# Kernel optimization log

Hardware: AMD Instinct MI355X
Metric: run time of the kernel (lower is better)

The kernel has to match this reference:

```python
import jax, jax.numpy as jnp
import numpy as np

NUM_SPARSE = 26
VOCAB = 100000
EMB = 64
B = 2048
DENSE = 13
NUM_FEA = NUM_SPARSE + 1  # 26 embeddings + bottom-MLP output


def _xavier(key, shape):
    fan_in, fan_out = shape[0], shape[1]
    lim = jnp.sqrt(6.0 / (fan_in + fan_out))
    return jax.random.uniform(key, shape, jnp.float32, -lim, lim)


def setup_inputs() -> dict:
    key = jax.random.key(0)
    ks = jax.random.split(key, 20)
    inp = {
        "dense": jax.random.normal(ks[0], (B, DENSE), jnp.float32),
        "cat_idx": jax.random.randint(ks[1], (B, NUM_SPARSE), 0, VOCAB, jnp.int32),
        # stacked EmbeddingBag tables (all same vocab -> one [26, V, 64] tensor)
        "tables": _xavier(ks[2], (VOCAB, EMB))[None] * jnp.ones((NUM_SPARSE, 1, 1), jnp.float32) * 0
                  + jax.random.normal(ks[3], (NUM_SPARSE, VOCAB, EMB), jnp.float32) * 0.01,
        # bottom MLP: 13 -> 512 -> 256 -> 64
        "bw0": _xavier(ks[4], (DENSE, 512)), "bb0": jnp.zeros((512,), jnp.float32),
        "bw1": _xavier(ks[5], (512, 256)),   "bb1": jnp.zeros((256,), jnp.float32),
        "bw2": _xavier(ks[6], (256, EMB)),   "bb2": jnp.zeros((EMB,), jnp.float32),
        # top MLP: 415 -> 1024 -> 512 -> 256 -> 1
        "tw0": _xavier(ks[7], (EMB + NUM_FEA * (NUM_FEA - 1) // 2, 1024)), "tb0": jnp.zeros((1024,), jnp.float32),
        "tw1": _xavier(ks[8], (1024, 512)),  "tb1": jnp.zeros((512,), jnp.float32),
        "tw2": _xavier(ks[9], (512, 256)),   "tb2": jnp.zeros((256,), jnp.float32),
        "tw3": _xavier(ks[10], (256, 1)),    "tb3": jnp.zeros((1,), jnp.float32),
    }
    return inp


def reference(dense, cat_idx, tables, bw0, bb0, bw1, bb1, bw2, bb2,
              tw0, tb0, tw1, tb1, tw2, tb2, tw3, tb3):
    # bottom MLP on dense features -> [B, EMB]
    h = jax.nn.relu(dense @ bw0 + bb0)
    h = jax.nn.relu(h @ bw1 + bb1)
    bot = jax.nn.relu(h @ bw2 + bb2)

    # EmbeddingBag (single index per bag, sum mode == plain gather): [B, 26, EMB]
    feat_ids = jnp.arange(NUM_SPARSE)[None, :]  # [1, 26]
    emb = tables[feat_ids, cat_idx]             # [B, 26, EMB]

    # dot interaction: batched Gram matrix then lower-triangular gather
    T = jnp.concatenate([bot[:, None, :], emb], axis=1)  # [B, 27, EMB]
    Z = jnp.einsum("bif,bjf->bij", T, T)                  # [B, 27, 27]
    li, lj = np.tril_indices(NUM_FEA, k=-1)               # 351 pairs
    Zflat = Z[:, li, lj]                                  # [B, 351]

    R = jnp.concatenate([bot, Zflat], axis=1)             # [B, 415]

    # top MLP
    r = jax.nn.relu(R @ tw0 + tb0)
    r = jax.nn.relu(r @ tw1 + tb1)
    r = jax.nn.relu(r @ tw2 + tb2)
    out = jax.nn.sigmoid(r @ tw3 + tb3)                   # [B, 1]
    return out
```

## Files before the change

kernel.cpp:

```cpp
#include <hip/hip_runtime.h>
#include <hip/hip_bf16.h>


#define BATCH 2048
#define VOCAB 100000
#define NSPARSE 26
#define NFEA 27
#define NPAIR 351
#define RLD 512

typedef __attribute__((ext_vector_type(8))) __bf16 bf16x8;
typedef __attribute__((ext_vector_type(4))) float f32x4;
typedef __hip_bfloat16 bf16;

#define GLOAD16(g, l)                                                          \
    __builtin_amdgcn_global_load_lds(                                          \
        (const __attribute__((address_space(1))) unsigned int*)(g),            \
        (__attribute__((address_space(3))) unsigned int*)(l), 16, 0, 0)

template<int BK>
__device__ __forceinline__ int swz(int row, int s) {
    return (BK == 128) ? (s ^ (row & 15))
         : (BK == 64)  ? (s ^ (row & 7))
                       : (s ^ ((row >> 1) & 3));
}

template<int BK, int WR, int WC, int MREP, int NREP, bool DENSEPAD>
__global__ __launch_bounds__(256) void gemm_bf16(
    const void* __restrict__ Araw,
    const bf16* __restrict__ Wt,
    const float* __restrict__ bias,
    bf16* __restrict__ C,
    int M, int N, int K, int ldC)
{
    constexpr int BM    = WR * MREP * 16;
    constexpr int BN    = WC * NREP * 16;
    constexpr int ROWB  = BK * 2;
    constexpr int SLOTS = BK / 8;
    constexpr int KKS   = BK / 32;
    constexpr int PA    = BM * SLOTS / 256;
    constexpr int PB    = BN * SLOTS / 256;

    __shared__ __align__(16) bf16 As[BM * BK];
    __shared__ __align__(16) bf16 Bs[BN * BK];

    const int t   = threadIdx.x;
    const int nbn = N / BN;
    const int bm  = blockIdx.x / nbn;
    const int bn  = blockIdx.x % nbn;
    const int row0 = bm * BM, n0 = bn * BN;

    const int wid  = t >> 6, lane = t & 63;
    const int wr   = wid / WC, wc = wid % WC;
    const int lr   = lane & 15;
    const int q    = lane >> 4;
    const int sslot = t % SLOTS;

    const bf16* Ab[PA];
    const bf16* Bb[PB];
#pragma unroll
    for (int p = 0; p < PA; ++p) {
        const int r = (p * 256 + t) / SLOTS;
        if (!DENSEPAD)
            Ab[p] = (const bf16*)Araw + (size_t)(row0 + r) * K +
                    swz<BK>(r, sslot) * 8;
    }
#pragma unroll
    for (int p = 0; p < PB; ++p) {
        const int r = (p * 256 + t) / SLOTS;
        Bb[p] = Wt + (size_t)(n0 + r) * K + swz<BK>(r, sslot) * 8;
    }

    f32x4 acc[MREP][NREP] = {};

    for (int k0 = 0; k0 < K; k0 += BK) {
        if constexpr (DENSEPAD) {
            const float* Df = (const float*)Araw;
#pragma unroll
            for (int idx = t; idx < BM * 32; idx += 256) {
                const int r = idx >> 5, c = idx & 31;
                const float v = (c < 13) ? Df[(size_t)(row0 + r) * 13 + c] : 0.f;
                As[r * 32 + swz<32>(r, c >> 3) * 8 + (c & 7)] =
                    __float2bfloat16(v);
            }
        } else {
#pragma unroll
            for (int p = 0; p < PA; ++p)
                GLOAD16(Ab[p] + k0, (char*)As + (p * 256 + t) * 16);
        }
#pragma unroll
        for (int p = 0; p < PB; ++p)
            GLOAD16(Bb[p] + k0, (char*)Bs + (p * 256 + t) * 16);
        __syncthreads();

        bf16x8 af[KKS][MREP], bfr[KKS][NREP];
#pragma unroll
        for (int kk = 0; kk < KKS; ++kk) {
#pragma unroll
            for (int m = 0; m < MREP; ++m) {
                const int r = wr * MREP * 16 + 16 * m + lr;
                af[kk][m] = *(const bf16x8*)((const char*)As + r * ROWB +
                                             swz<BK>(r, kk * 4 + q) * 16);
            }
#pragma unroll
            for (int n = 0; n < NREP; ++n) {
                const int r = wc * NREP * 16 + 16 * n + lr;
                bfr[kk][n] = *(const bf16x8*)((const char*)Bs + r * ROWB +
                                              swz<BK>(r, kk * 4 + q) * 16);
            }
        }
#pragma unroll
        for (int kk = 0; kk < KKS; ++kk)
#pragma unroll
            for (int m = 0; m < MREP; ++m)
#pragma unroll
                for (int n = 0; n < NREP; ++n)
                    acc[m][n] = __builtin_amdgcn_mfma_f32_16x16x32_bf16(
                        af[kk][m], bfr[kk][n], acc[m][n], 0, 0, 0);
        __syncthreads();
    }

#pragma unroll
    for (int n = 0; n < NREP; ++n) {
        const int col = n0 + wc * NREP * 16 + 16 * n + lr;
        const float bv = bias[col];
#pragma unroll
        for (int m = 0; m < MREP; ++m) {
#pragma unroll
            for (int i = 0; i < 4; ++i) {
                const int row = row0 + wr * MREP * 16 + 16 * m + q * 4 + i;
                float v = fmaxf(acc[m][n][i] + bv, 0.f);
                C[(size_t)row * ldC + col] = __float2bfloat16(v);
            }
        }
    }
}

__global__ __launch_bounds__(256) void top2_kernel(
    const bf16* __restrict__ A,
    const bf16* __restrict__ Wt,
    const float* __restrict__ bias,
    const float* __restrict__ w3,
    const float* __restrict__ b3,
    float* __restrict__ out)
{
    constexpr int BK = 64, BM = 32, K = 512;
    constexpr int SLOTS = 8, KKS = 2, PA = 1, PB = 8;

    __shared__ __align__(16) bf16 As[BM * BK];
    __shared__ __align__(16) bf16 Bs[256 * BK];
    __shared__ float rsum[BM];

    const int t = threadIdx.x;
    const int row0 = blockIdx.x * BM;
    const int wc = t >> 6, lane = t & 63;
    const int lr = lane & 15, q = lane >> 4;
    const int sslot = t % SLOTS;

    const bf16* Ab[PA];
    const bf16* Bb[PB];
#pragma unroll
    for (int p = 0; p < PA; ++p) {
        const int r = (p * 256 + t) / SLOTS;
        Ab[p] = A + (size_t)(row0 + r) * K + swz<BK>(r, sslot) * 8;
    }
#pragma unroll
    for (int p = 0; p < PB; ++p) {
        const int r = (p * 256 + t) / SLOTS;
        Bb[p] = Wt + (size_t)r * K + swz<BK>(r, sslot) * 8;
    }

    f32x4 acc[2][4] = {};

    for (int k0 = 0; k0 < K; k0 += BK) {
#pragma unroll
        for (int p = 0; p < PA; ++p)
            GLOAD16(Ab[p] + k0, (char*)As + (p * 256 + t) * 16);
#pragma unroll
        for (int p = 0; p < PB; ++p)
            GLOAD16(Bb[p] + k0, (char*)Bs + (p * 256 + t) * 16);
        __syncthreads();

        bf16x8 af[KKS][2], bfr[KKS][4];
#pragma unroll
        for (int kk = 0; kk < KKS; ++kk) {
#pragma unroll
            for (int m = 0; m < 2; ++m) {
                const int r = 16 * m + lr;
                af[kk][m] = *(const bf16x8*)((const char*)As + r * 128 +
                                             swz<BK>(r, kk * 4 + q) * 16);
            }
#pragma unroll
            for (int n = 0; n < 4; ++n) {
                const int r = wc * 64 + 16 * n + lr;
                bfr[kk][n] = *(const bf16x8*)((const char*)Bs + r * 128 +
                                              swz<BK>(r, kk * 4 + q) * 16);
            }
        }
#pragma unroll
        for (int kk = 0; kk < KKS; ++kk)
#pragma unroll
            for (int m = 0; m < 2; ++m)
#pragma unroll
                for (int n = 0; n < 4; ++n)
                    acc[m][n] = __builtin_amdgcn_mfma_f32_16x16x32_bf16(
                        af[kk][m], bfr[kk][n], acc[m][n], 0, 0, 0);
        __syncthreads();
    }

    if (t < BM) rsum[t] = 0.f;
    __syncthreads();

#pragma unroll
    for (int m = 0; m < 2; ++m) {
#pragma unroll
        for (int i = 0; i < 4; ++i) {
            float val = 0.f;
#pragma unroll
            for (int n = 0; n < 4; ++n) {
                const int col = wc * 64 + 16 * n + lr;
                val += fmaxf(acc[m][n][i] + bias[col], 0.f) * w3[col];
            }
            val += __shfl_xor(val, 1);
            val += __shfl_xor(val, 2);
            val += __shfl_xor(val, 4);
            val += __shfl_xor(val, 8);
            if (lr == 0) atomicAdd(&rsum[16 * m + q * 4 + i], val);
        }
    }
    __syncthreads();
    if (t < BM)
        out[row0 + t] = 1.f / (1.f + expf(-(rsum[t] + b3[0])));
}

struct WConvArgs {
    const float* src[6];
    bf16*        dst[6];
    int K[6], N[6], Kp[6], t0[7];
};

__global__ __launch_bounds__(256) void wconv_kernel(WConvArgs a)
{
    __shared__ float Ts[32][33];
    int w = 0;
    while (w < 5 && (int)blockIdx.x >= a.t0[w + 1]) ++w;
    const int rel = blockIdx.x - a.t0[w];
    const int K = a.K[w], N = a.N[w], Kp = a.Kp[w];
    const int nbn = N >> 5;
    const int tk = rel / nbn, tn = rel % nbn;
    const int tx = threadIdx.x & 31, ty = threadIdx.x >> 5;

    const float* src = a.src[w];
    bf16* dst = a.dst[w];

#pragma unroll
    for (int rr = 0; rr < 4; ++rr) {
        const int k = tk * 32 + ty + rr * 8;
        const int n = tn * 32 + tx;
        Ts[ty + rr * 8][tx] = (k < K) ? src[(size_t)k * N + n] : 0.f;
    }
    __syncthreads();
#pragma unroll
    for (int rr = 0; rr < 4; ++rr) {
        const int n = tn * 32 + ty + rr * 8;
        const int kp = tk * 32 + tx;
        dst[(size_t)n * Kp + kp] = __float2bfloat16(Ts[tx][ty + rr * 8]);
    }
}

__global__ __launch_bounds__(256) void interact_kernel(
    const int* __restrict__ cat_idx, const float* __restrict__ tables,
    bf16* __restrict__ R)
{
    __shared__ float T[NFEA][64 + 1];

    const int b    = blockIdx.x;
    const int t    = threadIdx.x;
    const int g    = t >> 6;
    const int lane = t & 63;
    bf16* Rrow = R + (size_t)b * RLD;

    for (int f = g; f < NFEA; f += 4) {
        if (f == 0) {
            T[0][lane] = __bfloat162float(Rrow[lane]);
        } else {
            const int j   = f - 1;
            const int idx = cat_idx[b * NSPARSE + j];
            T[f][lane] = tables[((size_t)j * VOCAB + idx) * 64 + lane];
        }
    }
    __syncthreads();

    if (t < RLD - 415) Rrow[415 + t] = __float2bfloat16(0.f);

    for (int p = t; p < NPAIR; p += 256) {
        int i = (int)((1.0f + sqrtf(1.0f + 8.0f * (float)p)) * 0.5f);
        while (i * (i - 1) / 2 > p) --i;
        while ((i + 1) * i / 2 <= p) ++i;
        const int j = p - i * (i - 1) / 2;
        float s = 0.f;
#pragma unroll 16
        for (int k = 0; k < 64; ++k) s += T[i][k] * T[j][k];
        Rrow[64 + p] = __float2bfloat16(s);
    }
}

extern "C" void kernel_launch(void* const* d_in, const int* in_sizes, int n_in,
                              void* d_out, int out_size, void* d_ws, size_t ws_size,
                              hipStream_t stream)
{
    const float* dense   = (const float*)d_in[0];
    const int*   cat_idx = (const int*)  d_in[1];
    const float* tables  = (const float*)d_in[2];
    const float* bw0 = (const float*)d_in[3];
    const float* bb0 = (const float*)d_in[4];
    const float* bw1 = (const float*)d_in[5];
    const float* bb1 = (const float*)d_in[6];
    const float* bw2 = (const float*)d_in[7];
    const float* bb2 = (const float*)d_in[8];
    const float* tw0 = (const float*)d_in[9];
    const float* tb0 = (const float*)d_in[10];
    const float* tw1 = (const float*)d_in[11];
    const float* tb1 = (const float*)d_in[12];
    const float* tw2 = (const float*)d_in[13];
    const float* tb2 = (const float*)d_in[14];
    const float* tw3 = (const float*)d_in[15];
    const float* tb3 = (const float*)d_in[16];

    bf16* p = (bf16*)d_ws;
    bf16* h0   = p; p += (size_t)BATCH * 512;
    bf16* h1   = p; p += (size_t)BATCH * 256;
    bf16* R    = p; p += (size_t)BATCH * RLD;
    bf16* r0   = p; p += (size_t)BATCH * 1024;
    bf16* r1   = p; p += (size_t)BATCH * 512;
    bf16* bw0t = p; p += 512 * 32;
    bf16* bw1t = p; p += 256 * 512;
    bf16* bw2t = p; p += 64 * 256;
    bf16* tw0t = p; p += 1024 * RLD;
    bf16* tw1t = p; p += 512 * 1024;
    bf16* tw2t = p; p += 256 * 512;
    float* out = (float*)d_out;

    WConvArgs wa;
    wa.src[0] = bw0;  wa.dst[0] = bw0t; wa.K[0] = 13;   wa.N[0] = 512;  wa.Kp[0] = 32;
    wa.src[1] = bw1;  wa.dst[1] = bw1t; wa.K[1] = 512;  wa.N[1] = 256;  wa.Kp[1] = 512;
    wa.src[2] = bw2;  wa.dst[2] = bw2t; wa.K[2] = 256;  wa.N[2] = 64;   wa.Kp[2] = 256;
    wa.src[3] = tw0;  wa.dst[3] = tw0t; wa.K[3] = 415;  wa.N[3] = 1024; wa.Kp[3] = RLD;
    wa.src[4] = tw1;  wa.dst[4] = tw1t; wa.K[4] = 1024; wa.N[4] = 512;  wa.Kp[4] = 1024;
    wa.src[5] = tw2;  wa.dst[5] = tw2t; wa.K[5] = 512;  wa.N[5] = 256;  wa.Kp[5] = 512;
    int tiles = 0;
    for (int w = 0; w < 6; ++w) {
        wa.t0[w] = tiles;
        tiles += (wa.Kp[w] >> 5) * (wa.N[w] >> 5);
    }
    wa.t0[6] = tiles;

    wconv_kernel<<<tiles, 256, 0, stream>>>(wa);

    gemm_bf16<32, 2, 2, 2, 2, true ><<<(BATCH / 64) * (512 / 64), 256, 0, stream>>>(
        dense, bw0t, bb0, h0, BATCH, 512, 32, 512);
    gemm_bf16<128, 2, 2, 1, 2, false><<<(BATCH / 32) * (256 / 64), 256, 0, stream>>>(
        h0, bw1t, bb1, h1, BATCH, 256, 512, 256);
    gemm_bf16<128, 2, 2, 1, 2, false><<<(BATCH / 32) * (64 / 64), 256, 0, stream>>>(
        h1, bw2t, bb2, R, BATCH, 64, 256, RLD);

    interact_kernel<<<BATCH, 256, 0, stream>>>(cat_idx, tables, R);

    gemm_bf16<128, 2, 2, 2, 2, false><<<(BATCH / 64) * (1024 / 64), 256, 0, stream>>>(
        R, tw0t, tb0, r0, BATCH, 1024, RLD, 1024);
    gemm_bf16<128, 2, 2, 1, 2, false><<<(BATCH / 32) * (512 / 64), 256, 0, stream>>>(
        r0, tw1t, tb1, r1, BATCH, 512, 1024, 512);
    top2_kernel<<<BATCH / 32, 256, 0, stream>>>(r1, tw2t, tb2, tw3, tb3, out);
}
```

Before: 59.70 us.

## Fuse three bottom-MLP GEMMs into one kernel keeping activations in LDS

Replaces the three separate bottom-MLP GEMM launches with a single kernel. Each block handles 8 batch rows, padded to 16 for MFMA, and keeps the intermediate activations h0 and h1 in swizzled shared memory, so they are never written to or read from global memory. This removes two kernel launches and the global round-trips of the intermediates. In exchange, half of each MFMA row tile is wasted on padding, and weights are read straight from global memory in every one of 256 blocks instead of being staged through LDS tiles.

```diff
diff --git a/kernel.cpp b/kernel.cpp
--- a/kernel.cpp
+++ b/kernel.cpp
@@ -13,6 +13,8 @@
 typedef __attribute__((ext_vector_type(4))) float f32x4;
 typedef __hip_bfloat16 bf16;
 
+#define MFMA16 __builtin_amdgcn_mfma_f32_16x16x32_bf16
+
 #define GLOAD16(g, l)                                                          \
     __builtin_amdgcn_global_load_lds(                                          \
         (const __attribute__((address_space(1))) unsigned int*)(g),            \
@@ -25,12 +27,115 @@
                        : (s ^ ((row >> 1) & 3));
 }
 
-template<int BK, int WR, int WC, int MREP, int NREP, bool DENSEPAD>
+__global__ __launch_bounds__(256) void bottom_kernel(
+    const float* __restrict__ dense,
+    const bf16* __restrict__ bw0t, const float* __restrict__ bb0,
+    const bf16* __restrict__ bw1t, const float* __restrict__ bb1,
+    const bf16* __restrict__ bw2t, const float* __restrict__ bb2,
+    bf16* __restrict__ R)
+{
+    __shared__ __align__(16) bf16 ds[16 * 32];
+    __shared__ __align__(16) bf16 h0s[16 * 512];
+    __shared__ __align__(16) bf16 h1s[16 * 256];
+
+    const int t   = threadIdx.x;
+    const int b0  = blockIdx.x * 8;
+    const int wid = t >> 6, lane = t & 63;
+    const int lr  = lane & 15, q = lane >> 4;
+
+    for (int idx = t; idx < 16 * 32; idx += 256) {
+        const int r = idx >> 5, c = idx & 31;
+        const float v = (r < 8 && c < 13) ? dense[(size_t)(b0 + r) * 13 + c] : 0.f;
+        ds[r * 32 + swz<32>(r, c >> 3) * 8 + (c & 7)] = __float2bfloat16(v);
+    }
+    __syncthreads();
+
+    {
+        const bf16x8 af = *(const bf16x8*)&ds[lr * 32 + swz<32>(lr, q) * 8];
+        const int n0 = wid * 128;
+        f32x4 acc[8] = {};
+#pragma unroll
+        for (int n = 0; n < 8; ++n) {
+            const bf16x8 bv =
+                *(const bf16x8*)(bw0t + (size_t)(n0 + n * 16 + lr) * 32 + q * 8);
+            acc[n] = MFMA16(af, bv, acc[n], 0, 0, 0);
+        }
+#pragma unroll
+        for (int n = 0; n < 8; ++n) {
+            const int col = n0 + n * 16 + lr;
+            const float bv = bb0[col];
+#pragma unroll
+            for (int i = 0; i < 4; ++i) {
+                const int row = q * 4 + i;
+                const float v = fmaxf(acc[n][i] + bv, 0.f);
+                h0s[row * 512 + (((col >> 3) ^ (row & 15)) << 3) + (col & 7)] =
+                    __float2bfloat16(v);
+            }
+        }
+    }
+    __syncthreads();
+
+    {
+        const int n0 = wid * 64;
+        const bf16* wp[4];
+#pragma unroll
+        for (int n = 0; n < 4; ++n)
+            wp[n] = bw1t + (size_t)(n0 + n * 16 + lr) * 512 + q * 8;
+
+        f32x4 acc[4] = {};
+#pragma unroll 4
+        for (int kk = 0; kk < 16; ++kk) {
+            const bf16x8 af = *(const bf16x8*)
+                &h0s[lr * 512 + (((kk * 4 + q) ^ (lr & 15)) << 3)];
+#pragma unroll
+            for (int n = 0; n < 4; ++n) {
+                const bf16x8 bv = *(const bf16x8*)(wp[n] + kk * 32);
+                acc[n] = MFMA16(af, bv, acc[n], 0, 0, 0);
+            }
+        }
+#pragma unroll
+        for (int n = 0; n < 4; ++n) {
+            const int col = n0 + n * 16 + lr;
+            const float bv = bb1[col];
+#pragma unroll
+            for (int i = 0; i < 4; ++i) {
+                const int row = q * 4 + i;
+                const float v = fmaxf(acc[n][i] + bv, 0.f);
+                h1s[row * 256 + (((col >> 3) ^ (row & 15)) << 3) + (col & 7)] =
+                    __float2bfloat16(v);
+            }
+        }
+    }
+    __syncthreads();
+
+    {
+        const int n0 = wid * 16;
+        const bf16* wp = bw2t + (size_t)(n0 + lr) * 256 + q * 8;
+        f32x4 acc = {};
+#pragma unroll
+        for (int kk = 0; kk < 8; ++kk) {
+            const bf16x8 af = *(const bf16x8*)
+                &h1s[lr * 256 + (((kk * 4 + q) ^ (lr & 15)) << 3)];
+            const bf16x8 bv = *(const bf16x8*)(wp + kk * 32);
+            acc = MFMA16(af, bv, acc, 0, 0, 0);
+        }
+        const int col = n0 + lr;
+        const float bv = bb2[col];
+#pragma unroll
+        for (int i = 0; i < 4; ++i) {
+            const int row = q * 4 + i;
+            if (row < 8) {
+                const float v = fmaxf(acc[i] + bv, 0.f);
+                R[(size_t)(b0 + row) * RLD + col] = __float2bfloat16(v);
+            }
+        }
+    }
+}
+
+template<int BK, int WR, int WC, int MREP, int NREP>
 __global__ __launch_bounds__(256) void gemm_bf16(
-    const void* __restrict__ Araw,
-    const bf16* __restrict__ Wt,
-    const float* __restrict__ bias,
-    bf16* __restrict__ C,
+    const bf16* __restrict__ A, const bf16* __restrict__ Wt,
+    const float* __restrict__ bias, bf16* __restrict__ C,
     int M, int N, int K, int ldC)
 {
     constexpr int BM    = WR * MREP * 16;
@@ -61,9 +166,7 @@
 #pragma unroll
     for (int p = 0; p < PA; ++p) {
         const int r = (p * 256 + t) / SLOTS;
-        if (!DENSEPAD)
-            Ab[p] = (const bf16*)Araw + (size_t)(row0 + r) * K +
-                    swz<BK>(r, sslot) * 8;
+        Ab[p] = A + (size_t)(row0 + r) * K + swz<BK>(r, sslot) * 8;
     }
 #pragma unroll
     for (int p = 0; p < PB; ++p) {
@@ -74,20 +177,9 @@
     f32x4 acc[MREP][NREP] = {};
 
     for (int k0 = 0; k0 < K; k0 += BK) {
-        if constexpr (DENSEPAD) {
-            const float* Df = (const float*)Araw;
-#pragma unroll
-            for (int idx = t; idx < BM * 32; idx += 256) {
-                const int r = idx >> 5, c = idx & 31;
-                const float v = (c < 13) ? Df[(size_t)(row0 + r) * 13 + c] : 0.f;
-                As[r * 32 + swz<32>(r, c >> 3) * 8 + (c & 7)] =
-                    __float2bfloat16(v);
-            }
-        } else {
-#pragma unroll
-            for (int p = 0; p < PA; ++p)
-                GLOAD16(Ab[p] + k0, (char*)As + (p * 256 + t) * 16);
-        }
+#pragma unroll
+        for (int p = 0; p < PA; ++p)
+            GLOAD16(Ab[p] + k0, (char*)As + (p * 256 + t) * 16);
 #pragma unroll
         for (int p = 0; p < PB; ++p)
             GLOAD16(Bb[p] + k0, (char*)Bs + (p * 256 + t) * 16);
@@ -115,8 +207,7 @@
             for (int m = 0; m < MREP; ++m)
 #pragma unroll
                 for (int n = 0; n < NREP; ++n)
-                    acc[m][n] = __builtin_amdgcn_mfma_f32_16x16x32_bf16(
-                        af[kk][m], bfr[kk][n], acc[m][n], 0, 0, 0);
+                    acc[m][n] = MFMA16(af[kk][m], bfr[kk][n], acc[m][n], 0, 0, 0);
         __syncthreads();
     }
 
@@ -137,12 +228,9 @@
 }
 
 __global__ __launch_bounds__(256) void top2_kernel(
-    const bf16* __restrict__ A,
-    const bf16* __restrict__ Wt,
-    const float* __restrict__ bias,
-    const float* __restrict__ w3,
-    const float* __restrict__ b3,
-    float* __restrict__ out)
+    const bf16* __restrict__ A, const bf16* __restrict__ Wt,
+    const float* __restrict__ bias, const float* __restrict__ w3,
+    const float* __restrict__ b3, float* __restrict__ out)
 {
     constexpr int BK = 64, BM = 32, K = 512;
     constexpr int SLOTS = 8, KKS = 2, PA = 1, PB = 8;
@@ -203,8 +291,7 @@
             for (int m = 0; m < 2; ++m)
 #pragma unroll
                 for (int n = 0; n < 4; ++n)
-                    acc[m][n] = __builtin_amdgcn_mfma_f32_16x16x32_bf16(
-                        af[kk][m], bfr[kk][n], acc[m][n], 0, 0, 0);
+                    acc[m][n] = MFMA16(af[kk][m], bfr[kk][n], acc[m][n], 0, 0, 0);
         __syncthreads();
     }
 
@@ -328,8 +415,6 @@
     const float* tb3 = (const float*)d_in[16];
 
     bf16* p = (bf16*)d_ws;
-    bf16* h0   = p; p += (size_t)BATCH * 512;
-    bf16* h1   = p; p += (size_t)BATCH * 256;
     bf16* R    = p; p += (size_t)BATCH * RLD;
     bf16* r0   = p; p += (size_t)BATCH * 1024;
     bf16* r1   = p; p += (size_t)BATCH * 512;
@@ -357,18 +442,14 @@
 
     wconv_kernel<<<tiles, 256, 0, stream>>>(wa);
 
-    gemm_bf16<32, 2, 2, 2, 2, true ><<<(BATCH / 64) * (512 / 64), 256, 0, stream>>>(
-        dense, bw0t, bb0, h0, BATCH, 512, 32, 512);
-    gemm_bf16<128, 2, 2, 1, 2, false><<<(BATCH / 32) * (256 / 64), 256, 0, stream>>>(
-        h0, bw1t, bb1, h1, BATCH, 256, 512, 256);
-    gemm_bf16<128, 2, 2, 1, 2, false><<<(BATCH / 32) * (64 / 64), 256, 0, stream>>>(
-        h1, bw2t, bb2, R, BATCH, 64, 256, RLD);
+    bottom_kernel<<<BATCH / 8, 256, 0, stream>>>(
+        dense, bw0t, bb0, bw1t, bb1, bw2t, bb2, R);
 
     interact_kernel<<<BATCH, 256, 0, stream>>>(cat_idx, tables, R);
 
-    gemm_bf16<128, 2, 2, 2, 2, false><<<(BATCH / 64) * (1024 / 64), 256, 0, stream>>>(
+    gemm_bf16<128, 2, 2, 2, 2><<<(BATCH / 64) * (1024 / 64), 256, 0, stream>>>(
         R, tw0t, tb0, r0, BATCH, 1024, RLD, 1024);
-    gemm_bf16<128, 2, 2, 1, 2, false><<<(BATCH / 32) * (512 / 64), 256, 0, stream>>>(
+    gemm_bf16<128, 2, 2, 1, 2><<<(BATCH / 32) * (512 / 64), 256, 0, stream>>>(
         r0, tw1t, tb1, r1, BATCH, 512, 1024, 512);
     top2_kernel<<<BATCH / 32, 256, 0, stream>>>(r1, tw2t, tb2, tw3, tb3, out);
 }
```

Result: no change. 59.86 us (+0.3%).
